# Performance work log

Measured on AMD Instinct MI355X. Metric: run time of the kernel, lower is better.

Reference implementation:

```python
import jax, jax.numpy as jnp
import numpy as np

CP, NP_, P = 32, 512, 2_000_000


def _grid_sample(plane, coords):
    """Bilinear grid_sample, align_corners=True, zeros padding.
    plane: [C,H,W]; coords: [P,2] in [-1,1] with (x->W, y->H). Returns [P,C]."""
    C, H, W = plane.shape
    x = (coords[:, 0] + 1.0) * 0.5 * (W - 1)
    y = (coords[:, 1] + 1.0) * 0.5 * (H - 1)
    x0 = jnp.floor(x)
    y0 = jnp.floor(y)
    wx1 = x - x0
    wy1 = y - y0

    def corner(xf, yf, w):
        xi = xf.astype(jnp.int32)
        yi = yf.astype(jnp.int32)
        valid = ((xi >= 0) & (xi < W) & (yi >= 0) & (yi < H)).astype(plane.dtype)
        xc = jnp.clip(xi, 0, W - 1)
        yc = jnp.clip(yi, 0, H - 1)
        return plane[:, yc, xc] * (w * valid)[None, :]  # [C,P]

    out = (corner(x0, y0, (1.0 - wx1) * (1.0 - wy1))
           + corner(x0 + 1.0, y0, wx1 * (1.0 - wy1))
           + corner(x0, y0 + 1.0, (1.0 - wx1) * wy1)
           + corner(x0 + 1.0, y0 + 1.0, wx1 * wy1))
    return out.T  # [P,C]


def setup_inputs() -> dict:
    key = jax.random.key(0)
    ks = jax.random.split(key, 9)
    rng, shift = 0.4, 0.1
    coordinates = jax.random.uniform(ks[0], (1, P, 3), jnp.float32, -1.0, 1.0)
    p0 = jax.random.uniform(ks[1], (CP, NP_, NP_), jnp.float32) * rng + shift
    p1 = jax.random.uniform(ks[2], (CP, NP_, NP_), jnp.float32) * rng + shift
    p2 = jax.random.uniform(ks[3], (CP, NP_, NP_), jnp.float32) * rng + shift
    W1 = jax.random.uniform(ks[4], (CP, 128), jnp.float32, -1.0, 1.0) / np.sqrt(CP)
    b1 = jax.random.uniform(ks[5], (128,), jnp.float32, -1.0, 1.0) / np.sqrt(CP)
    W2 = jax.random.uniform(ks[6], (128, 1), jnp.float32, -1.0, 1.0) / np.sqrt(128)
    b2 = jax.random.uniform(ks[7], (1,), jnp.float32, -1.0, 1.0) / np.sqrt(128)
    return {"coordinates": coordinates, "p0": p0, "p1": p1, "p2": p2,
            "W1": W1, "b1": b1, "W2": W2, "b2": b2}


def reference(coordinates, p0, p1, p2, W1, b1, W2, b2):
    c = coordinates[0]  # [P,3] (batch fixed at 1, matching plane batch)
    xy = _grid_sample(p0, c[:, 0:2])
    yz = _grid_sample(p1, c[:, 1:3])
    xz = _grid_sample(p2, c[:, ::2])
    feats = xy * yz * xz  # [P,Cp]
    h = jax.nn.relu(feats)
    h = jax.nn.relu(h @ W1 + b1)
    out = h @ W2 + b2  # [P,1]
    return out[None]  # [1,P,1]
```

## Files before the change

### kernel.cpp

```cpp
#include <hip/hip_runtime.h>
#include <hip/hip_fp16.h>
#include <cstdint>
#include <cstddef>

#define HH 512
#define WW 512
#define PLANE_H2 (512 * 512 * 16)
#define PLANE_BYTES (1 << 24)
#define NTILE (3 * 512 * 8)

typedef _Float16 f16x8 __attribute__((ext_vector_type(8)));
typedef float    f32x4 __attribute__((ext_vector_type(4)));

__device__ __forceinline__ float4 ldco(const float* __restrict__ coords,
                                       int g, int pl15, int P, int nG) {
    int gg = min(g, nG - 1);
    int pc = min((gg << 4) + pl15, P - 1);
    return *(const float4*)(coords + (size_t)pc * 3);
}

__device__ __forceinline__ void issue_slot(const char* __restrict__ trb,
                                           float4 cc, int kb,
                                           float* wx, float* wy, f16x8* q) {
    float cx = cc.x, cy = cc.y, cz = cc.z;
#pragma unroll
    for (int pl = 0; pl < 3; ++pl) {
        float u = (pl == 1) ? cy : cx;
        float v = (pl == 0) ? cy : cz;
        float xf = (u + 1.0f) * (0.5f * 511.0f);
        float yf = (v + 1.0f) * (0.5f * 511.0f);
        float x0f = floorf(xf), y0f = floorf(yf);
        wx[pl] = xf - x0f;
        wy[pl] = yf - y0f;
        int x0 = min(max((int)x0f, 0), 510);
        int y0 = min(max((int)y0f, 0), 510);
        const char* bp = trb + ((size_t)pl * PLANE_BYTES) +
                         ((size_t)(y0 * WW + x0) * 64 + kb * 16);
        q[pl * 4 + 0] = *(const f16x8*)(bp);
        q[pl * 4 + 1] = *(const f16x8*)(bp + 64);
        q[pl * 4 + 2] = *(const f16x8*)(bp + WW * 64);
        q[pl * 4 + 3] = *(const f16x8*)(bp + WW * 64 + 64);
    }
}

__device__ __forceinline__ void compute_store(
    const f16x8* q, const float* wx, const float* wy,
    const _Float16* __restrict__ W1h,
    const float* b1r, const float* w2r, float b2v,
    float* __restrict__ out, int pbase, int P, int kb, int pl15) {
    float s[8];
#pragma unroll
    for (int pl = 0; pl < 3; ++pl) {
        float w11 = wx[pl] * wy[pl];
        float w01 = wx[pl] - w11;
        float w10 = wy[pl] - w11;
        float w00 = 1.0f - wx[pl] - w10;
#pragma unroll
        for (int e = 0; e < 8; ++e) {
            float smp = (float)q[pl * 4 + 0][e] * w00 + (float)q[pl * 4 + 1][e] * w01 +
                        (float)q[pl * 4 + 2][e] * w10 + (float)q[pl * 4 + 3][e] * w11;
            s[e] = (pl == 0) ? smp : s[e] * smp;
        }
    }
    f16x8 af;
#pragma unroll
    for (int e = 0; e < 8; ++e) af[e] = (_Float16)fmaxf(s[e], 0.0f);

    float sum0 = 0.f, sum1 = 0.f, sum2 = 0.f, sum3 = 0.f;
#pragma unroll
    for (int hf = 0; hf < 2; ++hf) {
        f32x4 a0 = {0.f, 0.f, 0.f, 0.f}, a1 = a0, a2 = a0, a3 = a0;
        int ntb = hf * 4;
        const f16x8* bp0 = (const f16x8*)&W1h[(16 * (ntb + 0) + pl15) * 40 + kb * 8];
        const f16x8* bp1 = (const f16x8*)&W1h[(16 * (ntb + 1) + pl15) * 40 + kb * 8];
        const f16x8* bp2 = (const f16x8*)&W1h[(16 * (ntb + 2) + pl15) * 40 + kb * 8];
        const f16x8* bp3 = (const f16x8*)&W1h[(16 * (ntb + 3) + pl15) * 40 + kb * 8];
        a0 = __builtin_amdgcn_mfma_f32_16x16x32_f16(af, *bp0, a0, 0, 0, 0);
        a1 = __builtin_amdgcn_mfma_f32_16x16x32_f16(af, *bp1, a1, 0, 0, 0);
        a2 = __builtin_amdgcn_mfma_f32_16x16x32_f16(af, *bp2, a2, 0, 0, 0);
        a3 = __builtin_amdgcn_mfma_f32_16x16x32_f16(af, *bp3, a3, 0, 0, 0);
#pragma unroll
        for (int r = 0; r < 4; ++r) {
            float h0 = fmaxf(a0[r] + b1r[ntb + 0], 0.0f);
            float h1 = fmaxf(a1[r] + b1r[ntb + 1], 0.0f);
            float h2 = fmaxf(a2[r] + b1r[ntb + 2], 0.0f);
            float h3 = fmaxf(a3[r] + b1r[ntb + 3], 0.0f);
            float v4 = h0 * w2r[ntb + 0] + h1 * w2r[ntb + 1] +
                       h2 * w2r[ntb + 2] + h3 * w2r[ntb + 3];
            if (r == 0) sum0 += v4;
            else if (r == 1) sum1 += v4;
            else if (r == 2) sum2 += v4;
            else sum3 += v4;
        }
    }
#pragma unroll
    for (int m = 1; m <= 8; m <<= 1) {
        sum0 += __shfl_xor(sum0, m, 64);
        sum1 += __shfl_xor(sum1, m, 64);
        sum2 += __shfl_xor(sum2, m, 64);
        sum3 += __shfl_xor(sum3, m, 64);
    }
    if (pl15 == 0) {
        int op = pbase + kb * 4;
        if (op + 3 < P) {
            float4 o = {sum0 + b2v, sum1 + b2v, sum2 + b2v, sum3 + b2v};
            *(float4*)(out + op) = o;
        } else {
            if (op + 0 < P) out[op + 0] = sum0 + b2v;
            if (op + 1 < P) out[op + 1] = sum1 + b2v;
            if (op + 2 < P) out[op + 2] = sum2 + b2v;
            if (op + 3 < P) out[op + 3] = sum3 + b2v;
        }
    }
}

__global__ __launch_bounds__(256, 3) void kp_main(
    const float* __restrict__ coords,
    const float* __restrict__ p0, const float* __restrict__ p1,
    const float* __restrict__ p2,
    const float* __restrict__ W1, const float* __restrict__ b1,
    const float* __restrict__ W2, const float* __restrict__ b2,
    float* __restrict__ out, int P,
    unsigned int* __restrict__ bar, __half2* __restrict__ tr)
{
    __shared__ __align__(16) char smem[10240];
    float    (*tileF)[65] = (float(*)[65])smem;
    _Float16* W1h         = (_Float16*)smem;
    int t  = threadIdx.x;
    int nb = gridDim.x;

    for (int bid = blockIdx.x; bid < NTILE; bid += nb) {
        int xb = bid & 7, y = (bid >> 3) & 511, pl = bid >> 12;
        const float* src = (pl == 0) ? p0 : ((pl == 1) ? p1 : p2);
        int xbase = xb * 64;
        __syncthreads();
        int x = t & 63, cq = t >> 6;
#pragma unroll
        for (int i = 0; i < 8; ++i) {
            int c = cq * 8 + i;
            tileF[c][x] = src[c * (HH * WW) + y * WW + xbase + x];
        }
        __syncthreads();
        int c2 = t & 15, xq = t >> 4;
        __half2* dst = tr + (size_t)pl * PLANE_H2 + ((size_t)y * WW + xbase) * 16;
#pragma unroll
        for (int i = 0; i < 4; ++i) {
            int xx = xq * 4 + i;
            dst[xx * 16 + c2] =
                __floats2half2_rn(tileF[2 * c2][xx], tileF[2 * c2 + 1][xx]);
        }
    }
    __syncthreads();

    for (int e = t; e < 4096; e += 256) {
        int j = e >> 5, k = e & 31;
        W1h[j * 40 + k] = (_Float16)W1[k * 128 + j];
    }

    __syncthreads();
    if (t == 0) {
        __threadfence();
        __hip_atomic_fetch_add(bar, 1u, __ATOMIC_ACQ_REL, __HIP_MEMORY_SCOPE_AGENT);
        long long t0 = wall_clock64();
        while (__hip_atomic_load(bar, __ATOMIC_ACQUIRE, __HIP_MEMORY_SCOPE_AGENT)
               < (unsigned)nb) {
            __builtin_amdgcn_s_sleep(8);
            if (wall_clock64() - t0 > 50000000LL) break;
        }
        __threadfence();
    }
    __syncthreads();

    int wave = t >> 6, lane = t & 63;
    int pl15 = lane & 15;
    int kb   = lane >> 4;
    const char* trb = (const char*)tr;

    float b1r[8], w2r[8];
#pragma unroll
    for (int nt = 0; nt < 8; ++nt) {
        b1r[nt] = b1[16 * nt + pl15];
        w2r[nt] = W2[16 * nt + pl15];
    }
    float b2v = b2[0];

    int wid = blockIdx.x * 4 + wave;
    int nw  = nb * 4;
    int nG  = (P + 15) >> 4;

    float4 cc0 = ldco(coords, wid, pl15, P, nG);
    float4 cc1 = ldco(coords, wid + nw, pl15, P, nG);
    float wxA[3], wyA[3], wxB[3], wyB[3];
    f16x8 qA[12], qB[12];

    int g = wid;
    if (g < nG) {
        issue_slot(trb, cc0, kb, wxA, wyA, qA);
        while (true) {
            issue_slot(trb, cc1, kb, wxB, wyB, qB);
            cc0 = ldco(coords, g + 2 * nw, pl15, P, nG);
            compute_store(qA, wxA, wyA, W1h, b1r, w2r, b2v, out, g << 4, P, kb, pl15);
            g += nw;
            if (g >= nG) break;

            issue_slot(trb, cc0, kb, wxA, wyA, qA);
            cc1 = ldco(coords, g + 2 * nw, pl15, P, nG);
            compute_store(qB, wxB, wyB, W1h, b1r, w2r, b2v, out, g << 4, P, kb, pl15);
            g += nw;
            if (g >= nG) break;
        }
    }
}

__global__ __launch_bounds__(256) void kp_direct(
    const float* __restrict__ coords,
    const float* __restrict__ p0, const float* __restrict__ p1,
    const float* __restrict__ p2,
    const float* __restrict__ W1, const float* __restrict__ b1,
    const float* __restrict__ W2, const float* __restrict__ b2,
    float* __restrict__ out, int P)
{
    __shared__ float feats[256][33];
    int t = threadIdx.x;
    int wave = t >> 6, lane = t & 63, c = lane & 31, xsel = lane >> 5;
    int pbase = blockIdx.x * 256;

    for (int i = 0; i < 64; ++i) {
        int p = pbase + i * 4 + wave;
        if (p < P) {
            float cx = coords[3 * p + 0];
            float cy = coords[3 * p + 1];
            float cz = coords[3 * p + 2];
            float f = 1.0f;
#pragma unroll
            for (int pl = 0; pl < 3; ++pl) {
                const float* plane = (pl == 0) ? p0 : ((pl == 1) ? p1 : p2);
                float u = (pl == 1) ? cy : cx;
                float v = (pl == 0) ? cy : cz;
                float xf = (u + 1.0f) * (0.5f * 511.0f);
                float yf = (v + 1.0f) * (0.5f * 511.0f);
                float x0f = floorf(xf), y0f = floorf(yf);
                float wx = xf - x0f, wy = yf - y0f;
                int x0 = min(max((int)x0f, 0), 510);
                int y0 = min(max((int)y0f, 0), 510);
                const float* bp = plane + (size_t)c * (HH * WW) +
                                  (size_t)y0 * WW + (x0 + xsel);
                float v0 = bp[0];
                float v1 = bp[WW];
                float wxl = xsel ? wx : (1.0f - wx);
                float sm = (v0 * (1.0f - wy) + v1 * wy) * wxl;
                sm += __shfl_xor(sm, 32, 64);
                f *= sm;
            }
            if (xsel == 0) feats[i * 4 + wave][c] = fmaxf(f, 0.0f);
        }
    }
    __syncthreads();
    int p = pbase + t;
    if (p < P) {
        float fr[32];
#pragma unroll
        for (int k = 0; k < 32; ++k) fr[k] = feats[t][k];
        float acc = b2[0];
#pragma unroll 4
        for (int j = 0; j < 128; ++j) {
            float a = b1[j];
#pragma unroll
            for (int k = 0; k < 32; ++k) a += fr[k] * W1[k * 128 + j];
            acc += fmaxf(a, 0.0f) * W2[j];
        }
        out[p] = acc;
    }
}

extern "C" void kernel_launch(void* const* d_in, const int* in_sizes, int n_in,
                              void* d_out, int out_size, void* d_ws, size_t ws_size,
                              hipStream_t stream) {
    const float* coords = (const float*)d_in[0];
    const float* p0 = (const float*)d_in[1];
    const float* p1 = (const float*)d_in[2];
    const float* p2 = (const float*)d_in[3];
    const float* W1 = (const float*)d_in[4];
    const float* b1 = (const float*)d_in[5];
    const float* W2 = (const float*)d_in[6];
    const float* b2 = (const float*)d_in[7];
    float* out = (float*)d_out;
    int P = in_sizes[0] / 3;

    const size_t tr_off = 512;
    const size_t need   = tr_off + (size_t)3 * PLANE_H2 * sizeof(__half2);

    if (ws_size >= need) {
        int dev = 0, nCU = 0, maxb = 0;
        hipGetDevice(&dev);
        hipDeviceGetAttribute(&nCU, hipDeviceAttributeMultiprocessorCount, dev);
        hipOccupancyMaxActiveBlocksPerMultiprocessor(&maxb, kp_main, 256, 0);
        if (nCU <= 0) nCU = 32;
        if (maxb <= 0) maxb = 1;
        int nblk = nCU * maxb;

        unsigned int* bar = (unsigned int*)d_ws;
        __half2* tr = (__half2*)((char*)d_ws + tr_off);
        hipMemsetAsync(d_ws, 0, 512, stream);
        kp_main<<<dim3(nblk), dim3(256), 0, stream>>>(
            coords, p0, p1, p2, W1, b1, W2, b2, out, P, bar, tr);
    } else {
        int nblk = (P + 255) / 256;
        kp_direct<<<dim3(nblk), dim3(256), 0, stream>>>(
            coords, p0, p1, p2, W1, b1, W2, b2, out, P);
    }
}
```

Baseline: 417.2 us.

## Bucket-sort sample points by spatial octant and assign buckets per XCD

```diff
diff --git a/kernel.cpp b/kernel.cpp
--- a/kernel.cpp
+++ b/kernel.cpp
@@ -8,15 +8,24 @@
 #define PLANE_H2 (512 * 512 * 16)
 #define PLANE_BYTES (1 << 24)
 #define NTILE (3 * 512 * 8)
+#define NBKT 64
 
 typedef _Float16 f16x8 __attribute__((ext_vector_type(8)));
 typedef float    f32x4 __attribute__((ext_vector_type(4)));
 
-__device__ __forceinline__ float4 ldco(const float* __restrict__ coords,
+__device__ __forceinline__ int key_of(float x, float y, float z) {
+    int qx = min(max((int)((x + 1.0f) * 255.5f), 0), 511) >> 7;
+    int qy = min(max((int)((y + 1.0f) * 255.5f), 0), 511) >> 7;
+    int qz = min(max((int)((z + 1.0f) * 255.5f), 0), 511) >> 7;
+    return ((qx >> 1) << 5) | ((qy >> 1) << 4) | ((qz >> 1) << 3) |
+           ((qx & 1) << 2) | ((qy & 1) << 1) | (qz & 1);
+}
+
+__device__ __forceinline__ float4 ldco(const float4* __restrict__ sc,
                                        int g, int pl15, int P, int nG) {
     int gg = min(g, nG - 1);
     int pc = min((gg << 4) + pl15, P - 1);
-    return *(const float4*)(coords + (size_t)pc * 3);
+    return sc[pc];
 }
 
 __device__ __forceinline__ void issue_slot(const char* __restrict__ trb,
@@ -44,10 +53,10 @@
 }
 
 __device__ __forceinline__ void compute_store(
-    const f16x8* q, const float* wx, const float* wy,
+    const f16x8* q, const float* wx, const float* wy, float ccw,
     const _Float16* __restrict__ W1h,
     const float* b1r, const float* w2r, float b2v,
-    float* __restrict__ out, int pbase, int P, int kb, int pl15) {
+    float* __restrict__ out, int kb, int pl15) {
     float s[8];
 #pragma unroll
     for (int pl = 0; pl < 3; ++pl) {
@@ -100,18 +109,33 @@
         sum2 += __shfl_xor(sum2, m, 64);
         sum3 += __shfl_xor(sum3, m, 64);
     }
+    int sb = (kb << 4) + kb * 4;
+    int i0 = __float_as_int(__shfl(ccw, sb + 0, 64));
+    int i1 = __float_as_int(__shfl(ccw, sb + 1, 64));
+    int i2 = __float_as_int(__shfl(ccw, sb + 2, 64));
+    int i3 = __float_as_int(__shfl(ccw, sb + 3, 64));
     if (pl15 == 0) {
-        int op = pbase + kb * 4;
-        if (op + 3 < P) {
-            float4 o = {sum0 + b2v, sum1 + b2v, sum2 + b2v, sum3 + b2v};
-            *(float4*)(out + op) = o;
-        } else {
-            if (op + 0 < P) out[op + 0] = sum0 + b2v;
-            if (op + 1 < P) out[op + 1] = sum1 + b2v;
-            if (op + 2 < P) out[op + 2] = sum2 + b2v;
-            if (op + 3 < P) out[op + 3] = sum3 + b2v;
-        }
-    }
+        out[i0] = sum0 + b2v;
+        out[i1] = sum1 + b2v;
+        out[i2] = sum2 + b2v;
+        out[i3] = sum3 + b2v;
+    }
+}
+
+__device__ __forceinline__ void dev_barrier(unsigned int* ctr, int nb, int t) {
+    __syncthreads();
+    if (t == 0) {
+        __threadfence();
+        __hip_atomic_fetch_add(ctr, 1u, __ATOMIC_ACQ_REL, __HIP_MEMORY_SCOPE_AGENT);
+        long long t0 = wall_clock64();
+        while (__hip_atomic_load(ctr, __ATOMIC_ACQUIRE, __HIP_MEMORY_SCOPE_AGENT)
+               < (unsigned)nb) {
+            __builtin_amdgcn_s_sleep(8);
+            if (wall_clock64() - t0 > 50000000LL) break;
+        }
+        __threadfence();
+    }
+    __syncthreads();
 }
 
 __global__ __launch_bounds__(256, 3) void kp_main(
@@ -121,11 +145,17 @@
     const float* __restrict__ W1, const float* __restrict__ b1,
     const float* __restrict__ W2, const float* __restrict__ b2,
     float* __restrict__ out, int P,
-    unsigned int* __restrict__ bar, __half2* __restrict__ tr)
+    unsigned int* __restrict__ bar, unsigned int* __restrict__ hist,
+    int* __restrict__ blkhist, float4* __restrict__ sc,
+    __half2* __restrict__ tr)
 {
     __shared__ __align__(16) char smem[10240];
     float    (*tileF)[65] = (float(*)[65])smem;
     _Float16* W1h         = (_Float16*)smem;
+    __shared__ int hcnt[NBKT];
+    __shared__ int hl_pref[NBKT];
+    __shared__ int psum4[4 * NBKT];
+    __shared__ int lcur[NBKT];
     int t  = threadIdx.x;
     int nb = gridDim.x;
 
@@ -150,26 +180,61 @@
                 __floats2half2_rn(tileF[2 * c2][xx], tileF[2 * c2 + 1][xx]);
         }
     }
-    __syncthreads();
-
+
+    if (t < NBKT) hcnt[t] = 0;
+    __syncthreads();
+    int nCh = (P + 255) >> 8;
+    for (int ch = blockIdx.x; ch < nCh; ch += nb) {
+        int i = (ch << 8) + t;
+        if (i < P) {
+            float x = coords[3 * i], y = coords[3 * i + 1], z = coords[3 * i + 2];
+            atomicAdd(&hcnt[key_of(x, y, z)], 1);
+        }
+    }
+    __syncthreads();
+    if (t < NBKT) {
+        blkhist[blockIdx.x * NBKT + t] = hcnt[t];
+        atomicAdd(&hist[t], (unsigned)hcnt[t]);
+    }
+
+    dev_barrier(&bar[0], nb, t);
+
+    if (t < NBKT) hl_pref[t] = (int)hist[t];
+    __syncthreads();
+    int pref = 0;
+    if (t < NBKT)
+        for (int k = 0; k < t; ++k) pref += hl_pref[k];
+    {
+        int key = t & (NBKT - 1), q = t >> 6;
+        int lo = (int)(((long long)q * blockIdx.x) >> 2);
+        int hi = (int)(((long long)(q + 1) * blockIdx.x) >> 2);
+        int sacc = 0;
+        for (int b = lo; b < hi; ++b) sacc += blkhist[b * NBKT + key];
+        psum4[t] = sacc;
+    }
+    __syncthreads();
+    if (t < NBKT)
+        lcur[t] = pref + psum4[t] + psum4[NBKT + t] +
+                  psum4[2 * NBKT + t] + psum4[3 * NBKT + t];
+    __syncthreads();
+
+    for (int ch = blockIdx.x; ch < nCh; ch += nb) {
+        int i = (ch << 8) + t;
+        if (i < P) {
+            float x = coords[3 * i], y = coords[3 * i + 1], z = coords[3 * i + 2];
+            int slot = atomicAdd(&lcur[key_of(x, y, z)], 1);
+            float4 v = {x, y, z, __int_as_float(i)};
+            sc[slot] = v;
+        }
+    }
+
+    __syncthreads();
     for (int e = t; e < 4096; e += 256) {
         int j = e >> 5, k = e & 31;
         W1h[j * 40 + k] = (_Float16)W1[k * 128 + j];
     }
 
-    __syncthreads();
-    if (t == 0) {
-        __threadfence();
-        __hip_atomic_fetch_add(bar, 1u, __ATOMIC_ACQ_REL, __HIP_MEMORY_SCOPE_AGENT);
-        long long t0 = wall_clock64();
-        while (__hip_atomic_load(bar, __ATOMIC_ACQUIRE, __HIP_MEMORY_SCOPE_AGENT)
-               < (unsigned)nb) {
-            __builtin_amdgcn_s_sleep(8);
-            if (wall_clock64() - t0 > 50000000LL) break;
-        }
-        __threadfence();
-    }
-    __syncthreads();
+    dev_barrier(&bar[16], nb, t);
 
     int wave = t >> 6, lane = t & 63;
     int pl15 = lane & 15;
@@ -184,30 +249,37 @@
     }
     float b2v = b2[0];
 
-    int wid = blockIdx.x * 4 + wave;
-    int nw  = nb * 4;
     int nG  = (P + 15) >> 4;
-
-    float4 cc0 = ldco(coords, wid, pl15, P, nG);
-    float4 cc1 = ldco(coords, wid + nw, pl15, P, nG);
+    int xcd = blockIdx.x & 7;
+    int lb  = blockIdx.x >> 3;
+    int nbs = (nb >> 3) + ((blockIdx.x & 7) < (nb & 7) ? 1 : 0);
+    int gs  = (int)(((long long)xcd * nG) >> 3);
+    int ge  = (int)(((long long)(xcd + 1) * nG) >> 3);
+    int nws = nbs * 4;
+
     float wxA[3], wyA[3], wxB[3], wyB[3];
     f16x8 qA[12], qB[12];
 
-    int g = wid;
-    if (g < nG) {
+    int g = gs + lb * 4 + wave;
+    if (g < ge) {
+        float4 cc0 = ldco(sc, g, pl15, P, nG);
+        float4 cc1 = ldco(sc, g + nws, pl15, P, nG);
         issue_slot(trb, cc0, kb, wxA, wyA, qA);
+        float cwA = cc0.w, cwB;
         while (true) {
             issue_slot(trb, cc1, kb, wxB, wyB, qB);
-            cc0 = ldco(coords, g + 2 * nw, pl15, P, nG);
-            compute_store(qA, wxA, wyA, W1h, b1r, w2r, b2v, out, g << 4, P, kb, pl15);
-            g += nw;
-            if (g >= nG) break;
+            cwB = cc1.w;
+            cc0 = ldco(sc, g + 2 * nws, pl15, P, nG);
+            compute_store(qA, wxA, wyA, cwA, W1h, b1r, w2r, b2v, out, kb, pl15);
+            g += nws;
+            if (g >= ge) break;
 
             issue_slot(trb, cc0, kb, wxA, wyA, qA);
-            cc1 = ldco(coords, g + 2 * nw, pl15, P, nG);
-            compute_store(qB, wxB, wyB, W1h, b1r, w2r, b2v, out, g << 4, P, kb, pl15);
-            g += nw;
-            if (g >= nG) break;
+            cwA = cc0.w;
+            cc1 = ldco(sc, g + 2 * nws, pl15, P, nG);
+            compute_store(qB, wxB, wyB, cwB, W1h, b1r, w2r, b2v, out, kb, pl15);
+            g += nws;
+            if (g >= ge) break;
         }
     }
 }
@@ -287,8 +359,10 @@
     float* out = (float*)d_out;
     int P = in_sizes[0] / 3;
 
-    const size_t tr_off = 512;
-    const size_t need   = tr_off + (size_t)3 * PLANE_H2 * sizeof(__half2);
+    const size_t bh_off = 512;
+    const size_t sc_off = bh_off + 1024 * NBKT * sizeof(int);
+    const size_t tr_off = (sc_off + (size_t)P * 16 + 255) & ~(size_t)255;
+    const size_t need   = tr_off + (size_t)3 * PLANE_BYTES;
 
     if (ws_size >= need) {
         int dev = 0, nCU = 0, maxb = 0;
@@ -298,12 +372,16 @@
         if (nCU <= 0) nCU = 32;
         if (maxb <= 0) maxb = 1;
         int nblk = nCU * maxb;
-
-        unsigned int* bar = (unsigned int*)d_ws;
-        __half2* tr = (__half2*)((char*)d_ws + tr_off);
+        if (nblk > 1024) nblk = 1024;
+
+        unsigned int* bar  = (unsigned int*)d_ws;
+        unsigned int* hist = (unsigned int*)((char*)d_ws + 256);
+        int*          bh   = (int*)((char*)d_ws + bh_off);
+        float4*       sc   = (float4*)((char*)d_ws + sc_off);
+        __half2*      tr   = (__half2*)((char*)d_ws + tr_off);
         hipMemsetAsync(d_ws, 0, 512, stream);
         kp_main<<<dim3(nblk), dim3(256), 0, stream>>>(
-            coords, p0, p1, p2, W1, b1, W2, b2, out, P, bar, tr);
+            coords, p0, p1, p2, W1, b1, W2, b2, out, P, bar, hist, bh, sc, tr);
     } else {
         int nblk = (P + 255) / 256;
         kp_direct<<<dim3(nblk), dim3(256), 0, stream>>>(
```

Result: slower. 443.3 us (+6.3%).
